# Kernel tuning notes

Hardware: AMD Instinct MI355X
Metric: run time of the kernel (lower is better)

Reference implementation:

```python
import math
import jax, jax.numpy as jnp
import numpy as np

B, T, C = 2, 2048, 1024
H, N1, N2, N3 = 16, 6, 4, 6
HD = C // H  # 64


def setup_inputs() -> dict:
    key = jax.random.key(0)
    k1, k2, k3 = jax.random.split(key, 3)
    return {
        "x": jax.random.normal(k1, (B, T, C), jnp.float32),
        "qkv_w": jax.random.normal(k2, (3 * C, C), jnp.float32) * (C ** -0.5),
        "proj_w": jax.random.normal(k3, (C, C), jnp.float32) * (C ** -0.5),
        "proj_b": jnp.zeros((C,), jnp.float32),
        "curvature": jnp.ones((1, N2, 1, 1), jnp.float32),
    }


def _rotary(T_, hd, dtype):
    inv_freq = 1.0 / (10000.0 ** (jnp.arange(0, hd, 2, dtype=jnp.float32) / hd))
    freqs = jnp.outer(jnp.arange(T_, dtype=jnp.float32), inv_freq)  # [T, hd/2]
    return jnp.cos(freqs)[None, :, None, :].astype(dtype), jnp.sin(freqs)[None, :, None, :].astype(dtype)


def _apply_rot(x, cos, sin):
    x1, x2 = x[..., : x.shape[-1] // 2], x[..., x.shape[-1] // 2 :]
    return jnp.concatenate([x1 * cos + x2 * sin, -x1 * sin + x2 * cos], axis=-1).astype(x.dtype)


def _causal_bias(L, S, dtype):
    mask = jnp.triu(jnp.ones((L, S), bool), k=1)
    return jnp.where(mask, jnp.asarray(-jnp.inf, dtype), jnp.asarray(0.0, dtype))


def _sdpa(q, k, v, scale):
    # q,k,v: [B,h,T,hd]
    scores = jnp.einsum("bhtd,bhsd->bhts", q, k) * scale + _causal_bias(q.shape[-2], k.shape[-2], q.dtype)
    return jnp.einsum("bhts,bhsd->bhtd", jax.nn.softmax(scores, axis=-1), v)


def _hyp_attn(q, k, v, curv):
    # Lorentz-model hyperbolic attention. project(x,k) = [sqrt(1/k+||x||^2), x];
    # d(u,v) = sqrt(1/k) * arccosh(-k * <u,v>_L), <u,v>_L = -u0 v0 + <u_s, v_s>.
    eps = 1e-6
    tq = jnp.sqrt(1.0 / curv + jnp.sum(q * q, axis=-1, keepdims=True))  # [B,h,T,1]
    tk = jnp.sqrt(1.0 / curv + jnp.sum(k * k, axis=-1, keepdims=True))  # [B,h,S,1]
    inner = jnp.einsum("bhtd,bhsd->bhts", q, k) - tq * jnp.swapaxes(tk, -1, -2)  # Lorentz inner [B,h,T,S]
    arg = jnp.maximum(-curv * inner, 1.0 + 1e-7)
    dis = jnp.sqrt(1.0 / curv) * jnp.arccosh(arg)
    scores = 1.0 / (eps + dis) + _causal_bias(q.shape[-2], k.shape[-2], q.dtype)
    return jnp.einsum("bhts,bhsd->bhtd", jax.nn.softmax(scores, axis=-1), v)


def reference(x, qkv_w, proj_w, proj_b, curvature):
    Bx, Tx, Cx = x.shape
    qkv = x @ qkv_w.T  # [B,T,3C]
    q, k, v = jnp.split(qkv, 3, axis=-1)
    q = q.reshape(Bx, Tx, H, HD)
    k = k.reshape(Bx, Tx, H, HD)
    v = v.reshape(Bx, Tx, H, HD)
    cos, sin = _rotary(Tx, HD, x.dtype)
    q = _apply_rot(q, cos, sin)
    k = _apply_rot(k, cos, sin)
    # -> [B,H,T,hd]
    q, k, v = (jnp.swapaxes(t, 1, 2) for t in (q, k, v))
    outs = []
    # euclidean heads
    outs.append(_sdpa(q[:, :N1], k[:, :N1], v[:, :N1], 1.0 / math.sqrt(HD)))
    # hyperbolic heads
    outs.append(_hyp_attn(q[:, N1 : N1 + N2], k[:, N1 : N1 + N2], v[:, N1 : N1 + N2], curvature))
    # spherical heads (cosine-sim attention, scale = sqrt(head_dim))
    qn = q[:, N1 + N2 :] / jnp.maximum(jnp.linalg.norm(q[:, N1 + N2 :], axis=-1, keepdims=True), 1e-12)
    kn = k[:, N1 + N2 :] / jnp.maximum(jnp.linalg.norm(k[:, N1 + N2 :], axis=-1, keepdims=True), 1e-12)
    outs.append(_sdpa(qn, kn, v[:, N1 + N2 :], math.sqrt(HD)))
    y = jnp.concatenate(outs, axis=1)  # [B,H,T,hd]
    y = jnp.swapaxes(y, 1, 2).reshape(Bx, Tx, Cx)
    return y @ proj_w.T + proj_b
```

## Files before the change

kernel.cpp:

```cpp
#include <hip/hip_runtime.h>
#include <stdint.h>
#include <math.h>


typedef __bf16 bf16x8 __attribute__((ext_vector_type(8)));
typedef float f32x4 __attribute__((ext_vector_type(4)));

static __device__ __forceinline__ float bf2f(unsigned short u) {
  union { unsigned int i; float f; } v; v.i = ((unsigned int)u) << 16; return v.f;
}
static __device__ __forceinline__ unsigned short f2bf(float f) {
  union { float f; unsigned int i; } v; v.f = f;
  unsigned int x = v.i;
  x += 0x7fffu + ((x >> 16) & 1u);
  return (unsigned short)(x >> 16);
}

static __device__ __forceinline__ void async_copy16(const void* gsrc, void* ldst) {
  auto* lp = reinterpret_cast<__attribute__((address_space(3))) unsigned int*>(
      reinterpret_cast<uintptr_t>(ldst));
  auto* gp = reinterpret_cast<const __attribute__((address_space(1))) unsigned int*>(
      reinterpret_cast<uintptr_t>(gsrc));
  __builtin_amdgcn_global_load_lds(gp, lp, 16, 0, 0);
}

template <int PAT>
__global__ __launch_bounds__(256) void split2(const float* __restrict__ in,
                                              unsigned short* __restrict__ out) {
  const int row = blockIdx.x;
  const int kq = threadIdx.x * 4;
  const f32x4 x = *(const f32x4*)(in + (size_t)row * 1024 + kq);
  unsigned short hi[4], lo[4];
#pragma unroll
  for (int i = 0; i < 4; ++i) {
    hi[i] = f2bf(x[i]);
    lo[i] = f2bf(x[i] - bf2f(hi[i]));
  }
  uint2 uh, ul;
  uh.x = (unsigned)hi[0] | ((unsigned)hi[1] << 16);
  uh.y = (unsigned)hi[2] | ((unsigned)hi[3] << 16);
  ul.x = (unsigned)lo[0] | ((unsigned)lo[1] << 16);
  ul.y = (unsigned)lo[2] | ((unsigned)lo[3] << 16);
  unsigned short* op = out + (size_t)row * 2048 + kq;
  *(uint2*)(op)        = uh;
  *(uint2*)(op + 1024) = PAT ? uh : ul;
}

__global__ __launch_bounds__(256) void split1(const float* __restrict__ in,
                                              unsigned short* __restrict__ out) {
  const int row = blockIdx.x;
  const int kq = threadIdx.x * 4;
  const f32x4 x = *(const f32x4*)(in + (size_t)row * 1024 + kq);
  uint2 uh;
  uh.x = (unsigned)f2bf(x[0]) | ((unsigned)f2bf(x[1]) << 16);
  uh.y = (unsigned)f2bf(x[2]) | ((unsigned)f2bf(x[3]) << 16);
  *(uint2*)(out + (size_t)row * 1024 + kq) = uh;
}

template <int HASBIAS>
__global__ __launch_bounds__(256) void gemm_bt2(
    const unsigned short* __restrict__ A, const unsigned short* __restrict__ Bm,
    float* __restrict__ C, const float* __restrict__ bias,
    int NX, int N_, int Kr) {
  alignas(16) __shared__ unsigned short smAh[128 * 64];
  alignas(16) __shared__ unsigned short smAl[128 * 64];
  alignas(16) __shared__ unsigned short smB [128 * 64];
  const int tid = threadIdx.x;
  const int lane = tid & 63;
  const int wvi = tid >> 6;
  const int wm = wvi >> 1, wn = wvi & 1;
  const int cpx = gridDim.x >> 3;
  const int wgid = ((int)blockIdx.x & 7) * cpx + ((int)blockIdx.x >> 3);
  const long m0 = (long)(wgid / NX) * 128, n0 = (long)(wgid % NX) * 128;
  const int K2w = Kr * 2;

  const f32x4 zero4 = {0.f, 0.f, 0.f, 0.f};
  f32x4 acc[4][4];
#pragma unroll
  for (int i = 0; i < 4; ++i)
#pragma unroll
    for (int j = 0; j < 4; ++j) acc[i][j] = zero4;

  int mrow[4], gg[4];
#pragma unroll
  for (int w = 0; w < 4; ++w) {
    int c = w * 256 + tid;
    mrow[w] = c >> 3;
    gg[w] = (c & 7) ^ ((c >> 3) & 7);
  }

  const int kTiles = Kr >> 6;
  for (int kt = 0; kt < kTiles; ++kt) {
    if (kt) __syncthreads();
    const int kb = kt << 6;
#pragma unroll
    for (int w = 0; w < 4; ++w) {
      const int c = w * 256 + tid;
      const size_t arow = (size_t)(m0 + mrow[w]) * K2w + kb + gg[w] * 8;
      async_copy16(A + arow,        (char*)smAh + c * 16);
      async_copy16(A + arow + Kr,   (char*)smAl + c * 16);
      async_copy16(Bm + (size_t)(n0 + mrow[w]) * Kr + kb + gg[w] * 8,
                   (char*)smB + c * 16);
    }
    __syncthreads();
#pragma unroll
    for (int ks = 0; ks < 2; ++ks) {
      bf16x8 afh[4], afl[4], bg[4];
#pragma unroll
      for (int i = 0; i < 4; ++i) {
        const int ra = wm * 64 + i * 16 + (lane & 15);
        const int ga = (ks * 4 + (lane >> 4)) ^ (ra & 7);
        afh[i] = *(const bf16x8*)((const char*)smAh + ra * 128 + ga * 16);
        afl[i] = *(const bf16x8*)((const char*)smAl + ra * 128 + ga * 16);
        const int rb = wn * 64 + i * 16 + (lane & 15);
        const int gb2 = (ks * 4 + (lane >> 4)) ^ (rb & 7);
        bg[i] = *(const bf16x8*)((const char*)smB + rb * 128 + gb2 * 16);
      }
#pragma unroll
      for (int i = 0; i < 4; ++i)
#pragma unroll
        for (int j = 0; j < 4; ++j) {
          acc[i][j] = __builtin_amdgcn_mfma_f32_16x16x32_bf16(afh[i], bg[j], acc[i][j], 0, 0, 0);
          acc[i][j] = __builtin_amdgcn_mfma_f32_16x16x32_bf16(afl[i], bg[j], acc[i][j], 0, 0, 0);
        }
    }
  }

  const int r0 = wm * 64 + (lane >> 4) * 4;
  const int c0 = wn * 64 + (lane & 15);
#pragma unroll
  for (int j = 0; j < 4; ++j) {
    const long col = n0 + c0 + j * 16;
    float bv = 0.f;
    if (HASBIAS) bv = bias[col];
#pragma unroll
    for (int i = 0; i < 4; ++i) {
#pragma unroll
      for (int r = 0; r < 4; ++r) {
        const long row = m0 + r0 + i * 16 + r;
        C[row * N_ + col] = acc[i][j][r] + bv;
      }
    }
  }
}

__global__ __launch_bounds__(256) void prep(
    const float* __restrict__ qkvf, unsigned short* __restrict__ Q2,
    unsigned short* __restrict__ K2, unsigned short* __restrict__ V2,
    float* __restrict__ qq, float* __restrict__ kk, const float* __restrict__ curvg) {
  __shared__ unsigned short Vl[64 * 66];
  const int tid = threadIdx.x;
  const int zz = blockIdx.x;
  const int ttile = zz & 31, bh = zz >> 5;
  const int b = bh >> 4, h = bh & 15;
  const int t0 = ttile * 64;
  const int tr = tid >> 2, seg = tid & 3;
  const int t = t0 + tr;
  const float* src = qkvf + ((size_t)(b * 2048 + t)) * 3072 + h * 64 + seg * 16;

  float qv[16], kv[16], vv[16];
#pragma unroll
  for (int c = 0; c < 4; ++c) {
    const f32x4 a  = *(const f32x4*)(src + c * 4);
    const f32x4 bb = *(const f32x4*)(src + 1024 + c * 4);
    const f32x4 cc = *(const f32x4*)(src + 2048 + c * 4);
#pragma unroll
    for (int e = 0; e < 4; ++e) { qv[c*4+e] = a[e]; kv[c*4+e] = bb[e]; vv[c*4+e] = cc[e]; }
  }
  float qr[16], kr[16];
#pragma unroll
  for (int e = 0; e < 16; ++e) {
    const int d = seg * 16 + e;
    const int i = d & 31;
    const float invf = exp2f(-0.41524101186109286f * (float)i);
    float sn, cs;
    sincosf((float)t * invf, &sn, &cs);
    const float qo = __shfl_xor(qv[e], 2, 64);
    const float ko = __shfl_xor(kv[e], 2, 64);
    qr[e] = (d < 32) ? (qv[e] * cs + qo * sn) : (qv[e] * cs - qo * sn);
    kr[e] = (d < 32) ? (kv[e] * cs + ko * sn) : (kv[e] * cs - ko * sn);
  }
  float sq = 0.f, sk = 0.f;
#pragma unroll
  for (int e = 0; e < 16; ++e) { sq += qr[e] * qr[e]; sk += kr[e] * kr[e]; }
  sq += __shfl_xor(sq, 1, 64); sq += __shfl_xor(sq, 2, 64);
  sk += __shfl_xor(sk, 1, 64); sk += __shfl_xor(sk, 2, 64);
  float qscale = 0.125f * 1.4426950408889634f;
  if (h >= 10) {
    const float rq = 1.0f / fmaxf(sqrtf(sq), 1e-12f);
    const float rk = 1.0f / fmaxf(sqrtf(sk), 1e-12f);
#pragma unroll
    for (int e = 0; e < 16; ++e) { qr[e] *= rq; kr[e] *= rk; }
    qscale = 8.0f * 1.4426950408889634f;
  } else if (h >= 6) {
    qscale = 1.0f;
  }
#pragma unroll
  for (int e = 0; e < 16; ++e) qr[e] *= qscale;
  if (seg == 0) {
    const int idx = b * 32768 + h * 2048 + t;
    float oq = sq, ok = sk;
    if (h >= 6 && h < 10) {
      const float invc = 1.0f / curvg[h - 6];
      oq = sqrtf(invc + sq);
      ok = sqrtf(invc + sk);
    }
    qq[idx] = oq;
    kk[idx] = ok;
  }
  const int st = seg >> 1;
  const int quadA = (seg * 2) & 3, quadB = (seg * 2 + 1) & 3;
  {
    unsigned int wh[8], wl[8];
#pragma unroll
    for (int p = 0; p < 8; ++p) {
      unsigned short h0 = f2bf(qr[2*p]), h1 = f2bf(qr[2*p+1]);
      unsigned short l0 = f2bf(qr[2*p] - bf2f(h0)), l1 = f2bf(qr[2*p+1] - bf2f(h1));
      wh[p] = (unsigned)h0 | ((unsigned)h1 << 16);
      wl[p] = (unsigned)l0 | ((unsigned)l1 << 16);
    }
    const int qi = (t >> 4) & 1, c15q = t & 15;
    unsigned short* qs = Q2 + ((size_t)bh * 64 + (t >> 5)) * 4096;
    const int fh = ((qi * 2 + st) * 2 + 0) * 512, fl = fh + 512;
    *(uint4*)(qs + fh + quadA * 128 + c15q * 8) = uint4{wh[0], wh[1], wh[2], wh[3]};
    *(uint4*)(qs + fh + quadB * 128 + c15q * 8) = uint4{wh[4], wh[5], wh[6], wh[7]};
    *(uint4*)(qs + fl + quadA * 128 + c15q * 8) = uint4{wl[0], wl[1], wl[2], wl[3]};
    *(uint4*)(qs + fl + quadB * 128 + c15q * 8) = uint4{wl[4], wl[5], wl[6], wl[7]};
#pragma unroll
    for (int p = 0; p < 8; ++p) {
      unsigned short h0 = f2bf(kr[2*p]), h1 = f2bf(kr[2*p+1]);
      wh[p] = (unsigned)h0 | ((unsigned)h1 << 16);
    }
    const int kj = (tr >> 4) & 3, c15k = tr & 15;
    unsigned short* ks = K2 + ((size_t)bh * 32 + ttile) * 4096;
    const int gh = (st * 4 + kj) * 512;
    *(uint4*)(ks + gh + quadA * 128 + c15k * 8) = uint4{wh[0], wh[1], wh[2], wh[3]};
    *(uint4*)(ks + gh + quadB * 128 + c15k * 8) = uint4{wh[4], wh[5], wh[6], wh[7]};
  }
#pragma unroll
  for (int e = 0; e < 16; ++e) Vl[(seg * 16 + e) * 66 + tr] = f2bf(vv[e]);
  __syncthreads();
  {
    const int d = tid >> 2, tch = (tid & 3) * 16;
    unsigned int wv2[8];
#pragma unroll
    for (int p = 0; p < 8; ++p) {
      const unsigned short a0 = Vl[d * 66 + tch + 2*p];
      const unsigned short a1 = Vl[d * 66 + tch + 2*p + 1];
      wv2[p] = (unsigned)a0 | ((unsigned)a1 << 16);
    }
    const int dj = d >> 4, c15v = d & 15;
    const int ks2 = tch >> 5;
    const int qvA = (tch >> 3) & 3, qvB = ((tch >> 3) + 1) & 3;
    unsigned short* vs = V2 + ((size_t)bh * 32 + ttile) * 4096 + (ks2 * 4 + dj) * 512;
    *(uint4*)(vs + qvA * 128 + c15v * 8) = uint4{wv2[0], wv2[1], wv2[2], wv2[3]};
    *(uint4*)(vs + qvB * 128 + c15v * 8) = uint4{wv2[4], wv2[5], wv2[6], wv2[7]};
  }
}

__global__ __launch_bounds__(256, 2) void attn_part(
    const unsigned short* __restrict__ Q2, const unsigned short* __restrict__ K2,
    const unsigned short* __restrict__ V2, const float* __restrict__ tqq,
    const float* __restrict__ tkk, const float* __restrict__ curvg,
    float* __restrict__ part) {
  const int tid = threadIdx.x;
  const int lane = tid & 63;
  const int wv = tid >> 6;
  const int quad = lane >> 4, c15 = lane & 15;
  const int z = blockIdx.x * 4 + wv;
  const int bh = z / 160;
  const int u = 159 - (z - bh * 160);
  int qw, ch;
  if (u < 16)      { qw = u; ch = 0; }
  else if (u < 48) { qw = 16 + ((u - 16) >> 1); ch = (u - 16) & 1; }
  else if (u < 96) { const int s2 = u - 48; const int q3 = s2 / 3; qw = 32 + q3; ch = s2 - 3 * q3; }
  else             { const int s2 = u - 96; qw = 48 + (s2 >> 2); ch = s2 & 3; }
  const int h = bh & 15;
  const int geom = (h < 6) ? 0 : ((h < 10) ? 1 : 2);
  const int qrow0 = qw * 32;
  const f32x4 zero4 = {0.f, 0.f, 0.f, 0.f};

  const unsigned short* qbase = Q2 + ((size_t)bh * 64 + qw) * 4096;
  bf16x8 qh[2][2], ql[2][2];
#pragma unroll
  for (int qi = 0; qi < 2; ++qi)
#pragma unroll
    for (int st = 0; st < 2; ++st) {
      const int f = ((qi * 2 + st) * 2) * 512 + lane * 8;
      qh[qi][st] = *(const bf16x8*)(qbase + f);
      ql[qi][st] = *(const bf16x8*)(qbase + f + 512);
    }

  float curv = 1.f, sic = 1.f;
  const float Moff = 4.0f;
  float tqs[2] = {0.f, 0.f};
  if (geom == 1) {
    curv = curvg[h - 6];
    sic = sqrtf(1.0f / curv);
#pragma unroll
    for (int qi = 0; qi < 2; ++qi)
      tqs[qi] = tqq[bh * 2048 + qrow0 + qi * 16 + c15];
  }

  const __bf16 one_b = (__bf16)1.0f;
  const bf16x8 ones = {one_b, one_b, one_b, one_b, one_b, one_b, one_b, one_b};

  const int iA = ((quad & 1) * 32 + c15) * 4;
  const int iB = iA + 64;
  const bool hiq = (quad >= 2);

  f32x4 o[2][4];
  f32x4 ol[2] = {zero4, zero4};
#pragma unroll
  for (int qi = 0; qi < 2; ++qi)
#pragma unroll
    for (int dj = 0; dj < 4; ++dj) o[qi][dj] = zero4;

  const int nkt = (qw >> 1) + 1;
  const int ktB = ch * 8;
  const int ktE = (ktB + 8 < nkt) ? (ktB + 8) : nkt;
  for (int kt = ktB; kt < ktE; ++kt) {
    const int kb = kt * 64;
    const unsigned short* kbase = K2 + ((size_t)bh * 32 + kt) * 4096;
    const unsigned short* vbase = V2 + ((size_t)bh * 32 + kt) * 4096;

    bf16x8 kf[2][4], vf[2][4];
#pragma unroll
    for (int st = 0; st < 2; ++st)
#pragma unroll
      for (int kj = 0; kj < 4; ++kj)
        kf[st][kj] = *(const bf16x8*)(kbase + (st * 4 + kj) * 512 + lane * 8);
#pragma unroll
    for (int ks2 = 0; ks2 < 2; ++ks2)
#pragma unroll
      for (int dj = 0; dj < 4; ++dj)
        vf[ks2][dj] = *(const bf16x8*)(vbase + (ks2 * 4 + dj) * 512 + lane * 8);
    f32x4 tk4[4];
    if (geom == 1) {
#pragma unroll
      for (int kj = 0; kj < 4; ++kj)
        tk4[kj] = *(const f32x4*)(tkk + bh * 2048 + kb + kj * 16 + quad * 4);
    }

    f32x4 s[2][4];
#pragma unroll
    for (int qi = 0; qi < 2; ++qi)
#pragma unroll
      for (int kj = 0; kj < 4; ++kj) s[qi][kj] = zero4;
    __builtin_amdgcn_s_setprio(1);
#pragma unroll
    for (int st = 0; st < 2; ++st) {
#pragma unroll
      for (int kj = 0; kj < 4; ++kj) {
#pragma unroll
        for (int qi = 0; qi < 2; ++qi) {
          s[qi][kj] = __builtin_amdgcn_mfma_f32_16x16x32_bf16(kf[st][kj], qh[qi][st], s[qi][kj], 0, 0, 0);
          s[qi][kj] = __builtin_amdgcn_mfma_f32_16x16x32_bf16(kf[st][kj], ql[qi][st], s[qi][kj], 0, 0, 0);
        }
      }
    }
    __builtin_amdgcn_s_setprio(0);

    const bool needmask = (kt == nkt - 1);
    unsigned pw[2][4][2];
#pragma unroll
    for (int qi = 0; qi < 2; ++qi) {
      const int qcol = qrow0 + qi * 16 + c15;
#pragma unroll
      for (int kj = 0; kj < 4; ++kj) {
        const int kloc = kb + kj * 16 + quad * 4;
        const f32x4 d4 = s[qi][kj];
        f32x4 p;
        if (geom == 1) {
          const float tq = tqs[qi];
#pragma unroll
          for (int r = 0; r < 4; ++r) {
            const float a = fmaxf(curv * (tq * tk4[kj][r] - d4[r]), 1.0f + 1e-7f);
            const float dis = sic * __logf(a + sqrtf(a * a - 1.0f));
            p[r] = __expf(__builtin_amdgcn_rcpf(1e-6f + dis) - Moff);
          }
        } else {
#pragma unroll
          for (int r = 0; r < 4; ++r) p[r] = exp2f(d4[r]);
        }
        if (needmask) {
#pragma unroll
          for (int r = 0; r < 4; ++r)
            if (kloc + r > qcol) p[r] = 0.0f;
        }
        union { float f; unsigned u2; } b0, b1, b2, b3;
        b0.f = p[0]; b1.f = p[1]; b2.f = p[2]; b3.f = p[3];
        pw[qi][kj][0] = (b0.u2 >> 16) | (b1.u2 & 0xffff0000u);
        pw[qi][kj][1] = (b2.u2 >> 16) | (b3.u2 & 0xffff0000u);
      }
    }

    __builtin_amdgcn_s_setprio(1);
#pragma unroll
    for (int ks2 = 0; ks2 < 2; ++ks2) {
      const int a = ks2 * 2, b2 = ks2 * 2 + 1;
#pragma unroll
      for (int qi = 0; qi < 2; ++qi) {
        const int w0A = __builtin_amdgcn_ds_bpermute(iA, (int)pw[qi][a][0]);
        const int w0B = __builtin_amdgcn_ds_bpermute(iA, (int)pw[qi][b2][0]);
        const int w1A = __builtin_amdgcn_ds_bpermute(iA, (int)pw[qi][a][1]);
        const int w1B = __builtin_amdgcn_ds_bpermute(iA, (int)pw[qi][b2][1]);
        const int w2A = __builtin_amdgcn_ds_bpermute(iB, (int)pw[qi][a][0]);
        const int w2B = __builtin_amdgcn_ds_bpermute(iB, (int)pw[qi][b2][0]);
        const int w3A = __builtin_amdgcn_ds_bpermute(iB, (int)pw[qi][a][1]);
        const int w3B = __builtin_amdgcn_ds_bpermute(iB, (int)pw[qi][b2][1]);
        union { uint4 u; bf16x8 v; } pf;
        pf.u.x = (unsigned)(hiq ? w0B : w0A);
        pf.u.y = (unsigned)(hiq ? w1B : w1A);
        pf.u.z = (unsigned)(hiq ? w2B : w2A);
        pf.u.w = (unsigned)(hiq ? w3B : w3A);
        const bf16x8 pfrag = pf.v;
        ol[qi] = __builtin_amdgcn_mfma_f32_16x16x32_bf16(ones, pfrag, ol[qi], 0, 0, 0);
#pragma unroll
        for (int dj = 0; dj < 4; ++dj)
          o[qi][dj] = __builtin_amdgcn_mfma_f32_16x16x32_bf16(vf[ks2][dj], pfrag, o[qi][dj], 0, 0, 0);
      }
    }
    __builtin_amdgcn_s_setprio(0);
  }

  float* slot = part + (size_t)(bh * 160 + u) * 2112;
#pragma unroll
  for (int qi = 0; qi < 2; ++qi)
#pragma unroll
    for (int dj = 0; dj < 4; ++dj)
      *(f32x4*)(slot + (qi * 4 + dj) * 256 + lane * 4) = o[qi][dj];
  if (quad == 0) {
#pragma unroll
    for (int qi = 0; qi < 2; ++qi)
      slot[2048 + qi * 16 + c15] = ol[qi][0];
  }
}

__global__ __launch_bounds__(256) void attn_reduce(
    const float* __restrict__ part, unsigned short* __restrict__ Ay) {
  __shared__ float Ol[4][32 * 65];
  const int tid = threadIdx.x;
  const int lane = tid & 63;
  const int wv = tid >> 6;
  float* Olw = &Ol[wv][0];
  const int quad = lane >> 4, c15 = lane & 15;
  const int z = blockIdx.x * 4 + wv, bh = z & 31, qw = 63 - (z >> 5);
  const int b = bh >> 4, h = bh & 15;
  const int G = qw >> 4;
  const int base = qw + 8 * G * (G - 1) + (qw & 15) * G;
  const float* slot0 = part + (size_t)(bh * 160 + base) * 2112;

  const f32x4 zero4 = {0.f, 0.f, 0.f, 0.f};
  f32x4 o[8];
  float ls[2] = {0.f, 0.f};
#pragma unroll
  for (int i = 0; i < 8; ++i) o[i] = zero4;
  for (int chv = 0; chv <= G; ++chv) {
    const float* sl = slot0 + chv * 2112;
#pragma unroll
    for (int i = 0; i < 8; ++i) o[i] += *(const f32x4*)(sl + i * 256 + lane * 4);
#pragma unroll
    for (int qi = 0; qi < 2; ++qi)
      ls[qi] += sl[2048 + qi * 16 + c15];
  }
#pragma unroll
  for (int qi = 0; qi < 2; ++qi) {
    const float invl = __builtin_amdgcn_rcpf(ls[qi]);
#pragma unroll
    for (int dj = 0; dj < 4; ++dj) {
      const f32x4 val = o[qi * 4 + dj] * invl;
#pragma unroll
      for (int r = 0; r < 4; ++r)
        Olw[(qi * 16 + c15) * 65 + dj * 16 + quad * 4 + r] = val[r];
    }
  }
  __syncthreads();
  const int row = lane >> 1, half = lane & 1;
  const float* rp = Olw + row * 65 + half * 32;
  unsigned int uh[16], ul2[16];
#pragma unroll
  for (int p = 0; p < 16; ++p) {
    const float v0 = rp[2 * p], v1 = rp[2 * p + 1];
    const unsigned short h0 = f2bf(v0), h1 = f2bf(v1);
    const unsigned short g0 = f2bf(v0 - bf2f(h0)), g1 = f2bf(v1 - bf2f(h1));
    uh[p] = (unsigned)h0 | ((unsigned)h1 << 16);
    ul2[p] = (unsigned)g0 | ((unsigned)g1 << 16);
  }
  unsigned short* yp = Ay + ((size_t)(b * 2048 + qw * 32 + row)) * 2048 + h * 64 + half * 32;
#pragma unroll
  for (int c = 0; c < 4; ++c) {
    *(uint4*)(yp + 8 * c)        = uint4{uh[4*c], uh[4*c+1], uh[4*c+2], uh[4*c+3]};
    *(uint4*)(yp + 1024 + 8 * c) = uint4{ul2[4*c], ul2[4*c+1], ul2[4*c+2], ul2[4*c+3]};
  }
}

extern "C" void kernel_launch(void* const* d_in, const int* in_sizes, int n_in,
                              void* d_out, int out_size, void* d_ws, size_t ws_size,
                              hipStream_t stream) {
  const float* x      = (const float*)d_in[0];
  const float* qkv_w  = (const float*)d_in[1];
  const float* proj_w = (const float*)d_in[2];
  const float* proj_b = (const float*)d_in[3];
  const float* curvature = (const float*)d_in[4];
  float* out = (float*)d_out;

  char* ws = (char*)d_ws;
  unsigned short* AX   = (unsigned short*)ws;
  unsigned short* BW1  = (unsigned short*)(ws + 16777216);
  float*          QKVF = (float*)(ws + 33554432);
  unsigned short* Q2   = (unsigned short*)ws;
  unsigned short* K2   = (unsigned short*)(ws + 16777216);
  unsigned short* V2   = (unsigned short*)(ws + 25165824);
  float*          PART = (float*)(ws + 33554432);
  unsigned short* BPW1 = (unsigned short*)(ws + 76808192);
  unsigned short* AY   = (unsigned short*)ws;
  float*          QQ   = (float*)(ws + 94371840);
  float*          KK   = (float*)(ws + 94633984);

  split2<0><<<4096, 256, 0, stream>>>(x, AX);
  split1<<<3072, 256, 0, stream>>>(qkv_w, BW1);

  gemm_bt2<0><<<768, 256, 0, stream>>>(AX, BW1, QKVF, nullptr, 24, 3072, 1024);

  prep<<<1024, 256, 0, stream>>>(QKVF, Q2, K2, V2, QQ, KK, curvature);

  split1<<<1024, 256, 0, stream>>>(proj_w, BPW1);

  attn_part<<<1280, 256, 0, stream>>>(Q2, K2, V2, QQ, KK, curvature, PART);

  attn_reduce<<<512, 256, 0, stream>>>(PART, AY);

  gemm_bt2<1><<<256, 256, 0, stream>>>(AY, BPW1, out, proj_b, 8, 1024, 1024);
}
```

Measured before the change: 278.3 us.

## Fuse attention partial and reduce kernels by dropping key-chunk split

Removes the split-K decomposition of causal attention: each wave now processes the full key range for its 32-row query tile and writes the normalized bf16 hi/lo output directly, eliminating the partial-sum buffer and the separate reduce kernel. This saves a launch and the round-trip of fp32 partials through global memory. In exchange, parallelism drops from 1280 to 512 blocks and work per wave becomes highly unbalanced (late query tiles iterate up to 32 key tiles), which can lengthen the tail. AY is moved to a separate workspace region so it no longer aliases Q2 while attention is still reading it.

```diff
diff --git a/kernel.cpp b/kernel.cpp
--- a/kernel.cpp
+++ b/kernel.cpp
@@ -262,20 +262,17 @@
     const unsigned short* __restrict__ Q2, const unsigned short* __restrict__ K2,
     const unsigned short* __restrict__ V2, const float* __restrict__ tqq,
     const float* __restrict__ tkk, const float* __restrict__ curvg,
-    float* __restrict__ part) {
+    unsigned short* __restrict__ Ay) {
+  __shared__ float Ol[4][32 * 65];
   const int tid = threadIdx.x;
   const int lane = tid & 63;
   const int wv = tid >> 6;
+  float* Olw = &Ol[wv][0];
   const int quad = lane >> 4, c15 = lane & 15;
   const int z = blockIdx.x * 4 + wv;
-  const int bh = z / 160;
-  const int u = 159 - (z - bh * 160);
-  int qw, ch;
-  if (u < 16)      { qw = u; ch = 0; }
-  else if (u < 48) { qw = 16 + ((u - 16) >> 1); ch = (u - 16) & 1; }
-  else if (u < 96) { const int s2 = u - 48; const int q3 = s2 / 3; qw = 32 + q3; ch = s2 - 3 * q3; }
-  else             { const int s2 = u - 96; qw = 48 + (s2 >> 2); ch = s2 & 3; }
-  const int h = bh & 15;
+  const int qw = 63 - (z >> 5);
+  const int bh = z & 31;
+  const int b = bh >> 4, h = bh & 15;
   const int geom = (h < 6) ? 0 : ((h < 10) ? 1 : 2);
   const int qrow0 = qw * 32;
   const f32x4 zero4 = {0.f, 0.f, 0.f, 0.f};
@@ -317,9 +314,7 @@
     for (int dj = 0; dj < 4; ++dj) o[qi][dj] = zero4;
 
   const int nkt = (qw >> 1) + 1;
-  const int ktB = ch * 8;
-  const int ktE = (ktB + 8 < nkt) ? (ktB + 8) : nkt;
-  for (int kt = ktB; kt < ktE; ++kt) {
+  for (int kt = 0; kt < nkt; ++kt) {
     const int kb = kt * 64;
     const unsigned short* kbase = K2 + ((size_t)bh * 32 + kt) * 4096;
     const unsigned short* vbase = V2 + ((size_t)bh * 32 + kt) * 4096;
@@ -424,58 +419,19 @@
     __builtin_amdgcn_s_setprio(0);
   }
 
-  float* slot = part + (size_t)(bh * 160 + u) * 2112;
-#pragma unroll
-  for (int qi = 0; qi < 2; ++qi)
-#pragma unroll
-    for (int dj = 0; dj < 4; ++dj)
-      *(f32x4*)(slot + (qi * 4 + dj) * 256 + lane * 4) = o[qi][dj];
-  if (quad == 0) {
-#pragma unroll
-    for (int qi = 0; qi < 2; ++qi)
-      slot[2048 + qi * 16 + c15] = ol[qi][0];
-  }
-}
-
-__global__ __launch_bounds__(256) void attn_reduce(
-    const float* __restrict__ part, unsigned short* __restrict__ Ay) {
-  __shared__ float Ol[4][32 * 65];
-  const int tid = threadIdx.x;
-  const int lane = tid & 63;
-  const int wv = tid >> 6;
-  float* Olw = &Ol[wv][0];
-  const int quad = lane >> 4, c15 = lane & 15;
-  const int z = blockIdx.x * 4 + wv, bh = z & 31, qw = 63 - (z >> 5);
-  const int b = bh >> 4, h = bh & 15;
-  const int G = qw >> 4;
-  const int base = qw + 8 * G * (G - 1) + (qw & 15) * G;
-  const float* slot0 = part + (size_t)(bh * 160 + base) * 2112;
-
-  const f32x4 zero4 = {0.f, 0.f, 0.f, 0.f};
-  f32x4 o[8];
-  float ls[2] = {0.f, 0.f};
-#pragma unroll
-  for (int i = 0; i < 8; ++i) o[i] = zero4;
-  for (int chv = 0; chv <= G; ++chv) {
-    const float* sl = slot0 + chv * 2112;
-#pragma unroll
-    for (int i = 0; i < 8; ++i) o[i] += *(const f32x4*)(sl + i * 256 + lane * 4);
-#pragma unroll
-    for (int qi = 0; qi < 2; ++qi)
-      ls[qi] += sl[2048 + qi * 16 + c15];
-  }
 #pragma unroll
   for (int qi = 0; qi < 2; ++qi) {
-    const float invl = __builtin_amdgcn_rcpf(ls[qi]);
+    const float invl = __builtin_amdgcn_rcpf(ol[qi][0]);
 #pragma unroll
     for (int dj = 0; dj < 4; ++dj) {
-      const f32x4 val = o[qi * 4 + dj] * invl;
+      const f32x4 val = o[qi][dj] * invl;
 #pragma unroll
       for (int r = 0; r < 4; ++r)
         Olw[(qi * 16 + c15) * 65 + dj * 16 + quad * 4 + r] = val[r];
     }
   }
   __syncthreads();
+
   const int row = lane >> 1, half = lane & 1;
   const float* rp = Olw + row * 65 + half * 32;
   unsigned int uh[16], ul2[16];
@@ -512,9 +468,8 @@
   unsigned short* Q2   = (unsigned short*)ws;
   unsigned short* K2   = (unsigned short*)(ws + 16777216);
   unsigned short* V2   = (unsigned short*)(ws + 25165824);
-  float*          PART = (float*)(ws + 33554432);
+  unsigned short* AY   = (unsigned short*)(ws + 33554432);
   unsigned short* BPW1 = (unsigned short*)(ws + 76808192);
-  unsigned short* AY   = (unsigned short*)ws;
   float*          QQ   = (float*)(ws + 94371840);
   float*          KK   = (float*)(ws + 94633984);
 
@@ -527,9 +482,7 @@
 
   split1<<<1024, 256, 0, stream>>>(proj_w, BPW1);
 
-  attn_part<<<1280, 256, 0, stream>>>(Q2, K2, V2, QQ, KK, curvature, PART);
-
-  attn_reduce<<<512, 256, 0, stream>>>(PART, AY);
+  attn_part<<<512, 256, 0, stream>>>(Q2, K2, V2, QQ, KK, curvature, AY);
 
   gemm_bt2<1><<<256, 256, 0, stream>>>(AY, BPW1, out, proj_b, 8, 1024, 1024);
 }
```

Result: slower. 310.3 us (+11.5%).
